# Optimization experiments

Hardware: AMD Instinct MI355X
Metric: run time of the kernel (lower is better)

## Reference

```python
import jax, jax.numpy as jnp
import numpy as np

B, T, C, H = 2, 2048, 1024, 16
HD = C // H          # head_dim = 64
HALF = HD // 2       # rope half dim = 32
ROPE_BASE = 10000.0


def _build_sin_cos(seq_len, half_dim, base=ROPE_BASE):
    # mirrors build_sin_cos: angles[t, i] = t * base^(-2i / (2*half_dim))
    pos = jnp.arange(seq_len, dtype=jnp.float32)[:, None]                     # [T,1]
    inv_freq = 1.0 / (base ** (jnp.arange(0, half_dim * 2, 2, dtype=jnp.float32) / (half_dim * 2)))
    angles = pos * inv_freq                                                   # [T, half]
    return jnp.sin(angles), jnp.cos(angles)


def setup_inputs() -> dict:
    key = jax.random.key(0)
    k1, k2, k3 = jax.random.split(key, 3)
    x = jax.random.normal(k1, (B, T, C), dtype=jnp.float32)
    # nn.Linear weights (stored as [out,in] in torch; we keep [in,out] for x @ W)
    Wqkv = jax.random.normal(k2, (C, 3 * C), dtype=jnp.float32) * (C ** -0.5)
    Wproj = jax.random.normal(k3, (C, C), dtype=jnp.float32) * (C ** -0.5)
    rope_sin, rope_cos = _build_sin_cos(T, HALF)
    return {"x": x, "Wqkv": Wqkv, "Wproj": Wproj, "rope_sin": rope_sin, "rope_cos": rope_cos}


def reference(x, Wqkv, Wproj, rope_sin, rope_cos):
    Bb, Tt, Cc = x.shape
    Hh = H
    hd = Cc // Hh
    # fused QKV projection, then per-head split (matches view(B,T,H,3*hd).split)
    qkv = (x @ Wqkv).reshape(Bb, Tt, Hh, 3 * hd)
    q, k, v = jnp.split(qkv, 3, axis=-1)                                      # each [B,T,H,hd]
    # RoPE (single device path: local slice == full range)
    s = rope_sin[:Tt][None, :, None, :].astype(x.dtype)                       # [1,T,1,half]
    c = rope_cos[:Tt][None, :, None, :].astype(x.dtype)

    def rot(t):
        t1, t2 = jnp.split(t, 2, axis=-1)
        return jnp.concatenate([t1 * c - t2 * s, t1 * s + t2 * c], axis=-1)

    q = rot(q)
    k = rot(k)
    # causal scaled dot-product attention (flash_attn default scale = hd^-0.5)
    scale = jnp.asarray(hd, x.dtype) ** -0.5
    scores = jnp.einsum('bqhd,bkhd->bhqk', q, k) * scale                      # [B,H,T,T]
    causal = jnp.tril(jnp.ones((Tt, Tt), dtype=bool))
    scores = jnp.where(causal, scores, jnp.finfo(x.dtype).min)
    probs = jax.nn.softmax(scores, axis=-1)
    attn = jnp.einsum('bhqk,bkhd->bqhd', probs, v).reshape(Bb, Tt, Cc)
    return attn @ Wproj
```

## Files before the change

kernel.cpp:

```cpp
#include <hip/hip_runtime.h>

#define Bb 2
#define Tt 2048
#define Cc_ 1024
#define Hh 16
#define HDd 64

typedef __attribute__((ext_vector_type(8))) short bf16x8;
typedef __attribute__((ext_vector_type(4))) float f32x4;
typedef __attribute__((ext_vector_type(4))) unsigned short u16x4;

__device__ __forceinline__ unsigned short f2bf(float f) {
  union { float f; unsigned int u; } v; v.f = f;
  unsigned int r = v.u + 0x7FFFu + ((v.u >> 16) & 1u);
  return (unsigned short)(r >> 16);
}
__device__ __forceinline__ float bf2f(unsigned short u) {
  union { unsigned int u; float f; } v; v.u = ((unsigned int)u) << 16;
  return v.f;
}
__device__ __forceinline__ f32x4 mfma16(bf16x8 a, bf16x8 b, f32x4 c) {
  return __builtin_amdgcn_mfma_f32_16x16x32_bf16(a, b, c, 0, 0, 0);
}
__device__ __forceinline__ void gl_lds16(const void* g, void* l) {
  auto* gp = reinterpret_cast<const __attribute__((address_space(1))) unsigned int*>(
      reinterpret_cast<unsigned long long>(g));
  auto* lp = reinterpret_cast<__attribute__((address_space(3))) unsigned int*>(
      reinterpret_cast<unsigned long long>(l));
  __builtin_amdgcn_global_load_lds(gp, lp, 16, 0, 0);
}

__global__ __launch_bounds__(256) void k_cvt(const float* __restrict__ in,
                                             unsigned short* __restrict__ out, int n4) {
  const int i = blockIdx.x * 256 + threadIdx.x;
  if (i >= n4) return;
  f32x4 v = ((const f32x4*)in)[i];
  u16x4 o;
  o[0] = f2bf(v[0]); o[1] = f2bf(v[1]); o[2] = f2bf(v[2]); o[3] = f2bf(v[3]);
  ((u16x4*)out)[i] = o;
}

__global__ __launch_bounds__(256) void k_tcvt(const float* __restrict__ in,
                                              unsigned short* __restrict__ out, int R, int Cc) {
  __shared__ float tile[32][33];
  const int c0 = blockIdx.x * 32, r0 = blockIdx.y * 32;
  const int tx = threadIdx.x, ty = threadIdx.y;
#pragma unroll
  for (int i = 0; i < 4; ++i)
    tile[ty + i * 8][tx] = in[(size_t)(r0 + ty + i * 8) * Cc + c0 + tx];
  __syncthreads();
#pragma unroll
  for (int i = 0; i < 4; ++i)
    out[(size_t)(c0 + ty + i * 8) * R + r0 + tx] = f2bf(tile[tx][ty + i * 8]);
}

template <bool OUT_BF16>
__global__ __launch_bounds__(256) void k_gemm(const unsigned short* __restrict__ A,
                                              const unsigned short* __restrict__ Bt,
                                              void* __restrict__ Cout, int M, int N, int K) {
  __shared__ unsigned short lA[128 * 64];
  __shared__ unsigned short lB[128 * 64];
  const int tid = threadIdx.x;
  const int lane = tid & 63, wid = tid >> 6;
  const int wr = wid >> 1, wc = wid & 1;
  const int bm = blockIdx.y * 128, bn = blockIdx.x * 128;
  const int l15 = lane & 15, l4 = lane >> 4;
  f32x4 acc[4][4];
#pragma unroll
  for (int i = 0; i < 4; ++i)
#pragma unroll
    for (int j = 0; j < 4; ++j) acc[i][j] = f32x4{0.f, 0.f, 0.f, 0.f};
  const int nk = K >> 6;
  for (int t = 0; t < nk; ++t) {
    const int k0 = t << 6;
    __syncthreads();
#pragma unroll
    for (int i = 0; i < 4; ++i) {
      const int slot = i * 256 + tid;
      const int row = slot >> 3, g = slot & 7;
      const int gs = (g ^ (row & 7)) * 8;
      gl_lds16(A + (size_t)(bm + row) * K + k0 + gs, &lA[slot * 8]);
      gl_lds16(Bt + (size_t)(bn + row) * K + k0 + gs, &lB[slot * 8]);
    }
    __syncthreads();
#pragma unroll
    for (int ks = 0; ks < 2; ++ks) {
      bf16x8 af[4], bfr[4];
#pragma unroll
      for (int mf = 0; mf < 4; ++mf) {
        const int row = wr * 64 + mf * 16 + l15;
        const int g = ks * 4 + l4;
        af[mf] = *(const bf16x8*)&lA[row * 64 + ((g ^ (row & 7)) * 8)];
      }
#pragma unroll
      for (int nf = 0; nf < 4; ++nf) {
        const int row = wc * 64 + nf * 16 + l15;
        const int g = ks * 4 + l4;
        bfr[nf] = *(const bf16x8*)&lB[row * 64 + ((g ^ (row & 7)) * 8)];
      }
#pragma unroll
      for (int mf = 0; mf < 4; ++mf)
#pragma unroll
        for (int nf = 0; nf < 4; ++nf)
          acc[mf][nf] = mfma16(af[mf], bfr[nf], acc[mf][nf]);
    }
  }
  const int rb = bm + wr * 64 + l4 * 4;
  const int cb = bn + wc * 64 + l15;
#pragma unroll
  for (int mf = 0; mf < 4; ++mf)
#pragma unroll
    for (int nf = 0; nf < 4; ++nf)
#pragma unroll
      for (int j = 0; j < 4; ++j) {
        const size_t idx = (size_t)(rb + mf * 16 + j) * N + cb + nf * 16;
        if (OUT_BF16)
          ((unsigned short*)Cout)[idx] = f2bf(acc[mf][nf][j]);
        else
          ((float*)Cout)[idx] = acc[mf][nf][j];
      }
}

__global__ __launch_bounds__(256) void k_gemm64(const unsigned short* __restrict__ A,
                                                const unsigned short* __restrict__ Bt,
                                                float* __restrict__ Cout, int M, int N, int K) {
  __shared__ unsigned short lA[128 * 64];
  __shared__ unsigned short lB[64 * 64];
  const int tid = threadIdx.x;
  const int lane = tid & 63, w = tid >> 6;
  const int bm = blockIdx.y * 128, bn = blockIdx.x * 64;
  const int l15 = lane & 15, l4 = lane >> 4;
  f32x4 acc[2][4];
#pragma unroll
  for (int i = 0; i < 2; ++i)
#pragma unroll
    for (int j = 0; j < 4; ++j) acc[i][j] = f32x4{0.f, 0.f, 0.f, 0.f};
  const int nk = K >> 6;
  for (int t = 0; t < nk; ++t) {
    const int k0 = t << 6;
    __syncthreads();
#pragma unroll
    for (int i = 0; i < 4; ++i) {
      const int slot = i * 256 + tid;
      const int row = slot >> 3, g = slot & 7;
      const int gs = (g ^ (row & 7)) * 8;
      gl_lds16(A + (size_t)(bm + row) * K + k0 + gs, &lA[slot * 8]);
    }
#pragma unroll
    for (int i = 0; i < 2; ++i) {
      const int slot = i * 256 + tid;
      const int row = slot >> 3, g = slot & 7;
      const int gs = (g ^ (row & 7)) * 8;
      gl_lds16(Bt + (size_t)(bn + row) * K + k0 + gs, &lB[slot * 8]);
    }
    __syncthreads();
#pragma unroll
    for (int ks = 0; ks < 2; ++ks) {
      bf16x8 af[2], bfr[4];
#pragma unroll
      for (int mf = 0; mf < 2; ++mf) {
        const int row = w * 32 + mf * 16 + l15;
        const int g = ks * 4 + l4;
        af[mf] = *(const bf16x8*)&lA[row * 64 + ((g ^ (row & 7)) * 8)];
      }
#pragma unroll
      for (int nf = 0; nf < 4; ++nf) {
        const int row = nf * 16 + l15;
        const int g = ks * 4 + l4;
        bfr[nf] = *(const bf16x8*)&lB[row * 64 + ((g ^ (row & 7)) * 8)];
      }
#pragma unroll
      for (int mf = 0; mf < 2; ++mf)
#pragma unroll
        for (int nf = 0; nf < 4; ++nf)
          acc[mf][nf] = mfma16(af[mf], bfr[nf], acc[mf][nf]);
    }
  }
  const int rb = bm + w * 32 + l4 * 4;
  const int cb = bn + l15;
#pragma unroll
  for (int mf = 0; mf < 2; ++mf)
#pragma unroll
    for (int nf = 0; nf < 4; ++nf)
#pragma unroll
      for (int j = 0; j < 4; ++j)
        Cout[(size_t)(rb + mf * 16 + j) * N + cb + nf * 16] = acc[mf][nf][j];
}

__global__ __launch_bounds__(256) void k_rope(const unsigned short* __restrict__ qkv,
                                              const float* __restrict__ rsin,
                                              const float* __restrict__ rcos,
                                              unsigned short* __restrict__ Q,
                                              unsigned short* __restrict__ K) {
  const int tid = blockIdx.x * 256 + threadIdx.x;
  const int d = tid & 31;
  const int t = (tid >> 5) & 2047;
  const int h = (tid >> 16) & 15;
  const int b = tid >> 20;
  const size_t rq = (size_t)(b * Tt + t) * 3072 + h * 192;
  const float q1 = bf2f(qkv[rq + d]), q2 = bf2f(qkv[rq + 32 + d]);
  const float k1 = bf2f(qkv[rq + 64 + d]), k2 = bf2f(qkv[rq + 96 + d]);
  const float s = rsin[t * 32 + d], c = rcos[t * 32 + d];
  const size_t ob = ((size_t)(b * Hh + h) * Tt + t) * 64 + d;
  const float qs = 0.125f * 1.44269504088896f;
  Q[ob] = f2bf((q1 * c - q2 * s) * qs);
  Q[ob + 32] = f2bf((q1 * s + q2 * c) * qs);
  K[ob] = f2bf(k1 * c - k2 * s);
  K[ob + 32] = f2bf(k1 * s + k2 * c);
}

__global__ __launch_bounds__(256) void k_vrep(const unsigned short* __restrict__ qkv,
                                              unsigned short* __restrict__ Vt) {
  __shared__ unsigned short tile[32][72];
  const int bh = blockIdx.y;
  const int t0 = blockIdx.x * 32;
  const int tx = threadIdx.x, ty = threadIdx.y;
  const int b = bh >> 4, h = bh & 15;
#pragma unroll
  for (int i = 0; i < 4; ++i) {
    const int trow = ty + i * 8;
    const size_t r = (size_t)(b * Tt + t0 + trow) * 3072 + h * 192 + 128;
    tile[trow][tx] = qkv[r + tx];
    tile[trow][tx + 32] = qkv[r + 32 + tx];
  }
  __syncthreads();
#pragma unroll
  for (int i = 0; i < 8; ++i) {
    const int d = ty + i * 8;
    Vt[((size_t)bh * 64 + d) * Tt + t0 + tx] = tile[tx][d];
  }
}

__global__ __launch_bounds__(256) void k_attn(const unsigned short* __restrict__ Q,
                                              const unsigned short* __restrict__ Kt,
                                              const unsigned short* __restrict__ Vt,
                                              unsigned short* __restrict__ Aout) {
  __shared__ unsigned short lK[2][64 * 64];
  __shared__ unsigned short lV[2][64 * 64];
  __shared__ unsigned short lP[4][16 * 64];
  const int bid = blockIdx.x;
  const int slot0 = bid >> 3;
  const int bh = (bid & 7) * 4 + (slot0 >> 4);
  const int bxq = slot0 & 15;
  const int b = bh >> 4, h = bh & 15;
  const int tid = threadIdx.x, lane = tid & 63, w = tid >> 6;
  const int l15 = lane & 15, l4 = lane >> 4;
  const unsigned short* Kbh = Kt + (size_t)bh * Tt * 64;
  const unsigned short* Vbh = Vt + (size_t)bh * 64 * Tt;
  unsigned short* lPw = lP[w];

#define STAGE(buf, tt)                                                     \
  {                                                                        \
    const int kv0s = (tt) * 64;                                            \
    _Pragma("unroll") for (int i = 0; i < 2; ++i) {                        \
      const int slot = i * 256 + tid;                                      \
      const int row = slot >> 3, g = slot & 7;                             \
      const int gs = (g ^ (row & 7)) * 8;                                  \
      gl_lds16(Kbh + (size_t)(kv0s + row) * 64 + gs, &lK[buf][slot * 8]);  \
      gl_lds16(Vbh + (size_t)row * Tt + kv0s + gs, &lV[buf][slot * 8]);    \
    }                                                                      \
  }

  for (int ph = 0; ph < 2; ++ph) {
    const int qt = ph ? bxq : (31 - bxq);
    const int qb = qt * 64;
    const size_t qoff = ((size_t)bh * Tt + qb + w * 16 + l15) * 64 + l4 * 8;
    const bf16x8 qf0 = *(const bf16x8*)&Q[qoff];
    const bf16x8 qf1 = *(const bf16x8*)&Q[qoff + 32];
    f32x4 o[4];
#pragma unroll
    for (int i = 0; i < 4; ++i) o[i] = f32x4{0.f, 0.f, 0.f, 0.f};
    float mrun = -1e30f, lrun = 0.f;
    const int nt = qt + 1;
    STAGE(0, 0);
    asm volatile("s_waitcnt vmcnt(0)" ::: "memory");
    __builtin_amdgcn_s_barrier();
    for (int t = 0; t < nt; ++t) {
      const int cur = t & 1;
      const bool more = (t + 1 < nt);
      if (more) STAGE(cur ^ 1, t + 1);
      const int kv0 = t * 64;
      f32x4 s[4];
#pragma unroll
      for (int i = 0; i < 4; ++i) s[i] = f32x4{0.f, 0.f, 0.f, 0.f};
      __builtin_amdgcn_s_setprio(1);
#pragma unroll
      for (int ks = 0; ks < 2; ++ks) {
        const bf16x8 qa = ks ? qf1 : qf0;
#pragma unroll
        for (int nf = 0; nf < 4; ++nf) {
          const int row = nf * 16 + l15;
          const int g = ks * 4 + l4;
          const bf16x8 kf = *(const bf16x8*)&lK[cur][row * 64 + ((g ^ (row & 7)) * 8)];
          s[nf] = mfma16(kf, qa, s[nf]);
        }
      }
      __builtin_amdgcn_s_setprio(0);
      if (t == nt - 1) {
#pragma unroll
        for (int nf = 0; nf < 4; ++nf)
#pragma unroll
          for (int j = 0; j < 4; ++j)
            if (nf * 16 + l4 * 4 + j > w * 16 + l15) s[nf][j] = -3e38f;
      }
      float mx = fmaxf(fmaxf(fmaxf(s[0][0], s[0][1]), fmaxf(s[0][2], s[0][3])),
                       fmaxf(fmaxf(s[1][0], s[1][1]), fmaxf(s[1][2], s[1][3])));
      mx = fmaxf(mx, fmaxf(fmaxf(fmaxf(s[2][0], s[2][1]), fmaxf(s[2][2], s[2][3])),
                           fmaxf(fmaxf(s[3][0], s[3][1]), fmaxf(s[3][2], s[3][3]))));
      mx = fmaxf(mx, __shfl_xor(mx, 16, 64));
      mx = fmaxf(mx, __shfl_xor(mx, 32, 64));
      const bool need = !__all(mx - mrun <= 8.0f);
      float mnew = mrun;
      if (need) mnew = fmaxf(mrun, mx);
      float ssum = 0.f;
#pragma unroll
      for (int nf = 0; nf < 4; ++nf) {
        u16x4 pk;
#pragma unroll
        for (int j = 0; j < 4; ++j) {
          const float p = exp2f(s[nf][j] - mnew);
          ssum += p;
          pk[j] = f2bf(p);
        }
        const int g0 = nf * 2 + (l4 >> 1);
        *(u16x4*)&lPw[l15 * 64 + ((g0 ^ (l15 & 7)) * 8) + (l4 & 1) * 4] = pk;
      }
      ssum += __shfl_xor(ssum, 16, 64);
      ssum += __shfl_xor(ssum, 32, 64);
      if (need) {
        const float alpha = exp2f(mrun - mnew);
        lrun = lrun * alpha + ssum;
        mrun = mnew;
        float aj[4];
#pragma unroll
        for (int j = 0; j < 4; ++j) aj[j] = __shfl(alpha, l4 * 4 + j, 64);
#pragma unroll
        for (int df = 0; df < 4; ++df)
#pragma unroll
          for (int j = 0; j < 4; ++j) o[df][j] *= aj[j];
      } else {
        lrun += ssum;
      }
      __builtin_amdgcn_s_setprio(1);
#pragma unroll
      for (int kb = 0; kb < 2; ++kb) {
        const bf16x8 pa = *(const bf16x8*)&lPw[l15 * 64 + (((kb * 4 + l4) ^ (l15 & 7)) * 8)];
#pragma unroll
        for (int df = 0; df < 4; ++df) {
          const int row = df * 16 + l15;
          const int g = kb * 4 + l4;
          const bf16x8 vb = *(const bf16x8*)&lV[cur][row * 64 + ((g ^ (row & 7)) * 8)];
          o[df] = mfma16(pa, vb, o[df]);
        }
      }
      __builtin_amdgcn_s_setprio(0);
      if (more) asm volatile("s_waitcnt vmcnt(0)" ::: "memory");
      __builtin_amdgcn_s_barrier();
    }
    const float rinv = 1.f / lrun;
    float lj[4];
#pragma unroll
    for (int j = 0; j < 4; ++j) lj[j] = __shfl(rinv, l4 * 4 + j, 64);
#pragma unroll
    for (int j = 0; j < 4; ++j) {
      const size_t rr = (size_t)(b * Tt + qb + w * 16 + l4 * 4 + j) * 1024 + h * 64 + l15;
#pragma unroll
      for (int df = 0; df < 4; ++df) Aout[rr + df * 16] = f2bf(o[df][j] * lj[j]);
    }
  }
#undef STAGE
}

extern "C" void kernel_launch(void* const* d_in, const int* in_sizes, int n_in,
                              void* d_out, int out_size, void* d_ws, size_t ws_size,
                              hipStream_t stream) {
  const float* x = (const float*)d_in[0];
  const float* Wqkv = (const float*)d_in[1];
  const float* Wproj = (const float*)d_in[2];
  const float* rsin = (const float*)d_in[3];
  const float* rcos = (const float*)d_in[4];
  float* out = (float*)d_out;
  char* ws = (char*)d_ws;
  unsigned short* xb = (unsigned short*)(ws);
  unsigned short* wqkvt = (unsigned short*)(ws + (size_t)(8 << 20));
  unsigned short* wprot = (unsigned short*)(ws + (size_t)(14 << 20));
  unsigned short* qkv = (unsigned short*)(ws + (size_t)(16 << 20));
  unsigned short* Q = (unsigned short*)(ws + (size_t)(40 << 20));
  unsigned short* K = (unsigned short*)(ws + (size_t)(48 << 20));
  unsigned short* Vt = (unsigned short*)(ws + (size_t)(56 << 20));
  unsigned short* attn = (unsigned short*)(ws + (size_t)(64 << 20));

  k_cvt<<<4096, 256, 0, stream>>>(x, xb, 1048576);
  k_tcvt<<<dim3(96, 32), dim3(32, 8), 0, stream>>>(Wqkv, wqkvt, 1024, 3072);
  k_tcvt<<<dim3(32, 32), dim3(32, 8), 0, stream>>>(Wproj, wprot, 1024, 1024);
  k_gemm<true><<<dim3(24, 32), 256, 0, stream>>>(xb, wqkvt, qkv, 4096, 3072, 1024);
  k_rope<<<8192, 256, 0, stream>>>(qkv, rsin, rcos, Q, K);
  k_vrep<<<dim3(64, 32), dim3(32, 8), 0, stream>>>(qkv, Vt);
  k_attn<<<512, 256, 0, stream>>>(Q, K, Vt, attn);
  k_gemm64<<<dim3(16, 32), 256, 0, stream>>>(attn, wprot, out, 4096, 1024, 1024);
}
```

Measured before the change: 197.5 us.

## Split attention to one q-tile per block, unroll KV loop, pack bf16 conversions

The attention kernel now launches twice as many blocks, each handling a single query tile instead of a paired heavy/light pair, with an XCD-aware mapping that interleaves long and short tiles. The KV loop is manually unrolled by two so buffer indices are compile-time constants, and LDS offsets are precomputed. The row-sum reduction across lanes is deferred to the end, and the probability conversion uses the packed v_cvt_pk_bf16_f32 instruction. A launch bound hint of 4 blocks per CU is added. The aim is better load balance and occupancy plus less per-iteration ALU work, at the cost of losing the built-in heavy/light pairing and reloading Q setup per block.

```diff
diff --git a/kernel.cpp b/kernel.cpp
--- a/kernel.cpp
+++ b/kernel.cpp
@@ -9,6 +9,7 @@
 typedef __attribute__((ext_vector_type(8))) short bf16x8;
 typedef __attribute__((ext_vector_type(4))) float f32x4;
 typedef __attribute__((ext_vector_type(4))) unsigned short u16x4;
+typedef __attribute__((ext_vector_type(2))) unsigned int u32x2;
 
 __device__ __forceinline__ unsigned short f2bf(float f) {
   union { float f; unsigned int u; } v; v.f = f;
@@ -18,6 +19,11 @@
 __device__ __forceinline__ float bf2f(unsigned short u) {
   union { unsigned int u; float f; } v; v.u = ((unsigned int)u) << 16;
   return v.f;
+}
+__device__ __forceinline__ unsigned int cvtpk(float lo, float hi) {
+  unsigned int r;
+  asm("v_cvt_pk_bf16_f32 %0, %1, %2" : "=v"(r) : "v"(lo), "v"(hi));
+  return r;
 }
 __device__ __forceinline__ f32x4 mfma16(bf16x8 a, bf16x8 b, f32x4 c) {
   return __builtin_amdgcn_mfma_f32_16x16x32_bf16(a, b, c, 0, 0, 0);
@@ -231,144 +237,148 @@
   }
 }
 
-__global__ __launch_bounds__(256) void k_attn(const unsigned short* __restrict__ Q,
-                                              const unsigned short* __restrict__ Kt,
-                                              const unsigned short* __restrict__ Vt,
-                                              unsigned short* __restrict__ Aout) {
-  __shared__ unsigned short lK[2][64 * 64];
-  __shared__ unsigned short lV[2][64 * 64];
-  __shared__ unsigned short lP[4][16 * 64];
+__global__ __launch_bounds__(256, 4) void k_attn(const unsigned short* __restrict__ Q,
+                                                 const unsigned short* __restrict__ Kt,
+                                                 const unsigned short* __restrict__ Vt,
+                                                 unsigned short* __restrict__ Aout) {
+  __shared__ unsigned short lK[2 * 64 * 64];
+  __shared__ unsigned short lV[2 * 64 * 64];
+  __shared__ unsigned short lP[4 * 16 * 64];
   const int bid = blockIdx.x;
-  const int slot0 = bid >> 3;
-  const int bh = (bid & 7) * 4 + (slot0 >> 4);
-  const int bxq = slot0 & 15;
+  const int xcd = bid & 7, ss = bid >> 3;
+  const int cc = ss & 31, kk = ss >> 5;
+  const int bh = xcd * 4 + kk;
+  const int c2 = (cc + ((kk & 2) ? 16 : 0)) & 31;
+  const int qt = (kk & 1) ? (31 - c2) : c2;
   const int b = bh >> 4, h = bh & 15;
   const int tid = threadIdx.x, lane = tid & 63, w = tid >> 6;
   const int l15 = lane & 15, l4 = lane >> 4;
+  const int qb = qt * 64;
   const unsigned short* Kbh = Kt + (size_t)bh * Tt * 64;
   const unsigned short* Vbh = Vt + (size_t)bh * 64 * Tt;
-  unsigned short* lPw = lP[w];
-
-#define STAGE(buf, tt)                                                     \
-  {                                                                        \
-    const int kv0s = (tt) * 64;                                            \
-    _Pragma("unroll") for (int i = 0; i < 2; ++i) {                        \
-      const int slot = i * 256 + tid;                                      \
-      const int row = slot >> 3, g = slot & 7;                             \
-      const int gs = (g ^ (row & 7)) * 8;                                  \
-      gl_lds16(Kbh + (size_t)(kv0s + row) * 64 + gs, &lK[buf][slot * 8]);  \
-      gl_lds16(Vbh + (size_t)row * Tt + kv0s + gs, &lV[buf][slot * 8]);    \
-    }                                                                      \
-  }
-
-  for (int ph = 0; ph < 2; ++ph) {
-    const int qt = ph ? bxq : (31 - bxq);
-    const int qb = qt * 64;
-    const size_t qoff = ((size_t)bh * Tt + qb + w * 16 + l15) * 64 + l4 * 8;
-    const bf16x8 qf0 = *(const bf16x8*)&Q[qoff];
-    const bf16x8 qf1 = *(const bf16x8*)&Q[qoff + 32];
-    f32x4 o[4];
-#pragma unroll
-    for (int i = 0; i < 4; ++i) o[i] = f32x4{0.f, 0.f, 0.f, 0.f};
-    float mrun = -1e30f, lrun = 0.f;
-    const int nt = qt + 1;
-    STAGE(0, 0);
-    asm volatile("s_waitcnt vmcnt(0)" ::: "memory");
-    __builtin_amdgcn_s_barrier();
-    for (int t = 0; t < nt; ++t) {
-      const int cur = t & 1;
-      const bool more = (t + 1 < nt);
-      if (more) STAGE(cur ^ 1, t + 1);
-      const int kv0 = t * 64;
-      f32x4 s[4];
-#pragma unroll
-      for (int i = 0; i < 4; ++i) s[i] = f32x4{0.f, 0.f, 0.f, 0.f};
-      __builtin_amdgcn_s_setprio(1);
-#pragma unroll
-      for (int ks = 0; ks < 2; ++ks) {
-        const bf16x8 qa = ks ? qf1 : qf0;
-#pragma unroll
-        for (int nf = 0; nf < 4; ++nf) {
-          const int row = nf * 16 + l15;
-          const int g = ks * 4 + l4;
-          const bf16x8 kf = *(const bf16x8*)&lK[cur][row * 64 + ((g ^ (row & 7)) * 8)];
-          s[nf] = mfma16(kf, qa, s[nf]);
-        }
-      }
-      __builtin_amdgcn_s_setprio(0);
-      if (t == nt - 1) {
-#pragma unroll
-        for (int nf = 0; nf < 4; ++nf)
-#pragma unroll
-          for (int j = 0; j < 4; ++j)
-            if (nf * 16 + l4 * 4 + j > w * 16 + l15) s[nf][j] = -3e38f;
-      }
-      float mx = fmaxf(fmaxf(fmaxf(s[0][0], s[0][1]), fmaxf(s[0][2], s[0][3])),
-                       fmaxf(fmaxf(s[1][0], s[1][1]), fmaxf(s[1][2], s[1][3])));
-      mx = fmaxf(mx, fmaxf(fmaxf(fmaxf(s[2][0], s[2][1]), fmaxf(s[2][2], s[2][3])),
-                           fmaxf(fmaxf(s[3][0], s[3][1]), fmaxf(s[3][2], s[3][3]))));
-      mx = fmaxf(mx, __shfl_xor(mx, 16, 64));
-      mx = fmaxf(mx, __shfl_xor(mx, 32, 64));
-      const bool need = !__all(mx - mrun <= 8.0f);
-      float mnew = mrun;
-      if (need) mnew = fmaxf(mrun, mx);
-      float ssum = 0.f;
-#pragma unroll
-      for (int nf = 0; nf < 4; ++nf) {
-        u16x4 pk;
-#pragma unroll
-        for (int j = 0; j < 4; ++j) {
-          const float p = exp2f(s[nf][j] - mnew);
-          ssum += p;
-          pk[j] = f2bf(p);
-        }
-        const int g0 = nf * 2 + (l4 >> 1);
-        *(u16x4*)&lPw[l15 * 64 + ((g0 ^ (l15 & 7)) * 8) + (l4 & 1) * 4] = pk;
-      }
-      ssum += __shfl_xor(ssum, 16, 64);
-      ssum += __shfl_xor(ssum, 32, 64);
-      if (need) {
-        const float alpha = exp2f(mrun - mnew);
-        lrun = lrun * alpha + ssum;
-        mrun = mnew;
-        float aj[4];
-#pragma unroll
-        for (int j = 0; j < 4; ++j) aj[j] = __shfl(alpha, l4 * 4 + j, 64);
-#pragma unroll
-        for (int df = 0; df < 4; ++df)
-#pragma unroll
-          for (int j = 0; j < 4; ++j) o[df][j] *= aj[j];
-      } else {
-        lrun += ssum;
-      }
-      __builtin_amdgcn_s_setprio(1);
-#pragma unroll
-      for (int kb = 0; kb < 2; ++kb) {
-        const bf16x8 pa = *(const bf16x8*)&lPw[l15 * 64 + (((kb * 4 + l4) ^ (l15 & 7)) * 8)];
-#pragma unroll
-        for (int df = 0; df < 4; ++df) {
-          const int row = df * 16 + l15;
-          const int g = kb * 4 + l4;
-          const bf16x8 vb = *(const bf16x8*)&lV[cur][row * 64 + ((g ^ (row & 7)) * 8)];
-          o[df] = mfma16(pa, vb, o[df]);
-        }
-      }
-      __builtin_amdgcn_s_setprio(0);
-      if (more) asm volatile("s_waitcnt vmcnt(0)" ::: "memory");
-      __builtin_amdgcn_s_barrier();
-    }
-    const float rinv = 1.f / lrun;
-    float lj[4];
-#pragma unroll
-    for (int j = 0; j < 4; ++j) lj[j] = __shfl(rinv, l4 * 4 + j, 64);
-#pragma unroll
-    for (int j = 0; j < 4; ++j) {
-      const size_t rr = (size_t)(b * Tt + qb + w * 16 + l4 * 4 + j) * 1024 + h * 64 + l15;
-#pragma unroll
-      for (int df = 0; df < 4; ++df) Aout[rr + df * 16] = f2bf(o[df][j] * lj[j]);
-    }
-  }
+
+  int fo[4][2];
+#pragma unroll
+  for (int a = 0; a < 4; ++a)
+#pragma unroll
+    for (int bb = 0; bb < 2; ++bb)
+      fo[a][bb] = ((a * 16 + l15) * 64 + (((bb * 4 + l4) ^ (l15 & 7)) * 8)) * 2;
+  int pwo[4];
+#pragma unroll
+  for (int nf = 0; nf < 4; ++nf)
+    pwo[nf] = (l15 * 64 + (((nf * 2 + (l4 >> 1)) ^ (l15 & 7)) * 8) + (l4 & 1) * 4) * 2;
+  char* const pB = (char*)lP + w * 2048;
+  char* const kB0 = (char*)lK;
+  char* const vB0 = (char*)lV;
+  const int rA = tid >> 3;
+  const int gsA = ((tid & 7) ^ (rA & 7)) * 8;
+  const int kgA = rA * 64 + gsA;
+  const int vgA = rA * 2048 + gsA;
+  char* const ldKA = (char*)lK + tid * 16;
+  char* const ldVA = (char*)lV + tid * 16;
+
+#define STAGE(BUF, TT)                                                   \
+  {                                                                      \
+    const int kv_ = (TT) * 64;                                           \
+    gl_lds16(Kbh + kv_ * 64 + kgA, ldKA + (BUF) * 8192);                 \
+    gl_lds16(Kbh + kv_ * 64 + kgA + 32 * 64, ldKA + (BUF) * 8192 + 4096);\
+    gl_lds16(Vbh + kv_ + vgA, ldVA + (BUF) * 8192);                      \
+    gl_lds16(Vbh + kv_ + vgA + 32 * 2048, ldVA + (BUF) * 8192 + 4096);   \
+  }
+
+  const size_t qoff = ((size_t)bh * Tt + qb + w * 16 + l15) * 64 + l4 * 8;
+  const bf16x8 qf0 = *(const bf16x8*)&Q[qoff];
+  const bf16x8 qf1 = *(const bf16x8*)&Q[qoff + 32];
+  f32x4 o[4];
+#pragma unroll
+  for (int i = 0; i < 4; ++i) o[i] = f32x4{0.f, 0.f, 0.f, 0.f};
+  float mrun = -1e30f, lrun = 0.f;
+  const int nt = qt + 1;
+
+#define BODY(CUR, T, LASTT)                                                       \
+  {                                                                               \
+    if ((T) + 1 < nt) STAGE(CUR ^ 1, (T) + 1);                                    \
+    f32x4 sv[4];                                                                  \
+    _Pragma("unroll") for (int i = 0; i < 4; ++i) sv[i] = f32x4{0.f, 0.f, 0.f, 0.f}; \
+    __builtin_amdgcn_s_setprio(1);                                                \
+    _Pragma("unroll") for (int ks = 0; ks < 2; ++ks) {                            \
+      const bf16x8 qa = ks ? qf1 : qf0;                                           \
+      _Pragma("unroll") for (int nf = 0; nf < 4; ++nf) {                          \
+        const bf16x8 kf = *(const bf16x8*)(kB0 + (CUR) * 8192 + fo[nf][ks]);      \
+        sv[nf] = mfma16(kf, qa, sv[nf]);                                          \
+      }                                                                           \
+    }                                                                             \
+    __builtin_amdgcn_s_setprio(0);                                                \
+    if (LASTT) {                                                                  \
+      _Pragma("unroll") for (int nf = 0; nf < 4; ++nf)                            \
+        _Pragma("unroll") for (int j = 0; j < 4; ++j)                             \
+          if (nf * 16 + l4 * 4 + j > w * 16 + l15) sv[nf][j] = -3e38f;            \
+    }                                                                             \
+    float mx = fmaxf(fmaxf(fmaxf(sv[0][0], sv[0][1]), fmaxf(sv[0][2], sv[0][3])), \
+                     fmaxf(fmaxf(sv[1][0], sv[1][1]), fmaxf(sv[1][2], sv[1][3])));\
+    mx = fmaxf(mx, fmaxf(fmaxf(fmaxf(sv[2][0], sv[2][1]), fmaxf(sv[2][2], sv[2][3])), \
+                         fmaxf(fmaxf(sv[3][0], sv[3][1]), fmaxf(sv[3][2], sv[3][3])))); \
+    if (!__all(mx - mrun <= 8.0f)) {                                              \
+      mx = fmaxf(mx, __shfl_xor(mx, 16, 64));                                     \
+      mx = fmaxf(mx, __shfl_xor(mx, 32, 64));                                     \
+      const float mnew = fmaxf(mrun, mx);                                         \
+      const float alpha = exp2f(mrun - mnew);                                     \
+      lrun *= alpha;                                                              \
+      float aj[4];                                                                \
+      _Pragma("unroll") for (int j = 0; j < 4; ++j) aj[j] = __shfl(alpha, l4 * 4 + j, 64); \
+      _Pragma("unroll") for (int df = 0; df < 4; ++df)                            \
+        _Pragma("unroll") for (int j = 0; j < 4; ++j) o[df][j] *= aj[j];          \
+      mrun = mnew;                                                                \
+    }                                                                             \
+    _Pragma("unroll") for (int nf = 0; nf < 4; ++nf) {                            \
+      const float p0 = exp2f(sv[nf][0] - mrun), p1 = exp2f(sv[nf][1] - mrun);     \
+      const float p2 = exp2f(sv[nf][2] - mrun), p3 = exp2f(sv[nf][3] - mrun);     \
+      lrun += (p0 + p1) + (p2 + p3);                                              \
+      u32x2 pk; pk[0] = cvtpk(p0, p1); pk[1] = cvtpk(p2, p3);                     \
+      *(u32x2*)(pB + pwo[nf]) = pk;                                               \
+    }                                                                             \
+    __builtin_amdgcn_s_setprio(1);                                                \
+    _Pragma("unroll") for (int kb = 0; kb < 2; ++kb) {                            \
+      const bf16x8 pa = *(const bf16x8*)(pB + fo[0][kb]);                         \
+      _Pragma("unroll") for (int df = 0; df < 4; ++df) {                          \
+        const bf16x8 vb = *(const bf16x8*)(vB0 + (CUR) * 8192 + fo[df][kb]);      \
+        o[df] = mfma16(pa, vb, o[df]);                                            \
+      }                                                                           \
+    }                                                                             \
+    __builtin_amdgcn_s_setprio(0);                                                \
+    if ((T) + 1 < nt) asm volatile("s_waitcnt vmcnt(0)" ::: "memory");            \
+    __builtin_amdgcn_s_barrier();                                                 \
+  }
+
+  STAGE(0, 0);
+  asm volatile("s_waitcnt vmcnt(0)" ::: "memory");
+  __builtin_amdgcn_s_barrier();
+  int t = 0;
+  for (; t + 2 < nt; t += 2) {
+    BODY(0, t, false);
+    BODY(1, t + 1, false);
+  }
+  if (nt - t == 2) {
+    BODY(0, t, false);
+    BODY(1, t + 1, true);
+  } else {
+    BODY(0, t, true);
+  }
+#undef BODY
 #undef STAGE
+
+  lrun += __shfl_xor(lrun, 16, 64);
+  lrun += __shfl_xor(lrun, 32, 64);
+  const float rinv = 1.f / lrun;
+  float lj[4];
+#pragma unroll
+  for (int j = 0; j < 4; ++j) lj[j] = __shfl(rinv, l4 * 4 + j, 64);
+#pragma unroll
+  for (int j = 0; j < 4; ++j) {
+    const size_t rr = (size_t)(b * Tt + qb + w * 16 + l4 * 4 + j) * 1024 + h * 64 + l15;
+#pragma unroll
+    for (int df = 0; df < 4; ++df) Aout[rr + df * 16] = f2bf(o[df][j] * lj[j]);
+  }
 }
 
 extern "C" void kernel_launch(void* const* d_in, const int* in_sizes, int n_in,
@@ -396,6 +406,6 @@
   k_gemm<true><<<dim3(24, 32), 256, 0, stream>>>(xb, wqkvt, qkv, 4096, 3072, 1024);
   k_rope<<<8192, 256, 0, stream>>>(qkv, rsin, rcos, Q, K);
   k_vrep<<<dim3(64, 32), dim3(32, 8), 0, stream>>>(qkv, Vt);
-  k_attn<<<512, 256, 0, stream>>>(Q, K, Vt, attn);
+  k_attn<<<1024, 256, 0, stream>>>(Q, K, Vt, attn);
   k_gemm64<<<dim3(16, 32), 256, 0, stream>>>(attn, wprot, out, 4096, 1024, 1024);
 }
```

After: 194.9 us. No clear change (-1.3%).
